# Optimization experiments

Hardware: AMD Instinct MI355X
Metric: run time of the kernel (lower is better)

The kernel has to match this reference:

```python
import jax, jax.numpy as jnp
import numpy as np
from jax import lax

B, N, D = 8, 16384, 64
NPOINT, NSAMPLE, RADIUS = 1024, 32, 0.1
MLP = [3 + D, 64, 64, 128]
BN_EPS = 1e-5


def setup_inputs() -> dict:
    key = jax.random.key(0)
    ks = jax.random.split(key, 8)
    inp = {
        'xyz': jax.random.uniform(ks[0], (B, 3, N), dtype=jnp.float32),
        'points': jax.random.normal(ks[1], (B, D, N), dtype=jnp.float32),
    }
    for i, (cin, cout) in enumerate(zip(MLP[:-1], MLP[1:]), start=1):
        inp[f'w{i}'] = jax.random.normal(ks[1 + i], (cout, cin), dtype=jnp.float32) / np.sqrt(cin)
        inp[f'b{i}'] = jnp.zeros((cout,), jnp.float32)
        inp[f'g{i}'] = jnp.ones((cout,), jnp.float32)
        inp[f'be{i}'] = jnp.zeros((cout,), jnp.float32)
    return inp


def farthest_point_sample(xyz, npoint):
    # xyz: (B, N, 3). Deterministic start at index 0 (torch uses randint).
    b, n, _ = xyz.shape

    def step(carry, _):
        distance, farthest = carry  # (B,N), (B,)
        centroid = jnp.take_along_axis(xyz, farthest[:, None, None], axis=1)  # (B,1,3)
        dist = jnp.sum((xyz - centroid) ** 2, axis=-1)  # (B,N)
        distance = jnp.minimum(distance, dist)
        new_far = jnp.argmax(distance, axis=-1).astype(jnp.int32)
        return (distance, new_far), farthest

    init = (jnp.full((b, n), 1e10, xyz.dtype), jnp.zeros((b,), jnp.int32))
    _, idxs = lax.scan(step, init, None, length=npoint)  # (npoint, B)
    return idxs.T  # (B, npoint)


def query_ball_point(radius, nsample, xyz, new_xyz):
    # xyz: (B,N,3), new_xyz: (B,S,3) -> (B,S,nsample) int32
    b, n, _ = xyz.shape
    # squared pairwise distances (B,S,N)
    sqr = (jnp.sum(new_xyz ** 2, -1)[:, :, None]
           + jnp.sum(xyz ** 2, -1)[:, None, :]
           - 2.0 * jnp.einsum('bsc,bnc->bsn', new_xyz, xyz))
    group_idx = jnp.where(sqr > radius ** 2, n, jnp.arange(n, dtype=jnp.int32))
    group_idx = jnp.sort(group_idx, axis=-1)[:, :, :nsample]
    first = group_idx[:, :, :1]
    return jnp.where(group_idx == n, first, group_idx)


def reference(xyz, points, w1, b1, g1, be1, w2, b2, g2, be2, w3, b3, g3, be3):
    xyz_t = xyz.transpose(0, 2, 1)      # (B,N,3)
    pts_t = points.transpose(0, 2, 1)   # (B,N,D)
    bsz = xyz_t.shape[0]

    fps_idx = farthest_point_sample(xyz_t, NPOINT)          # (B,S)
    bidx2 = jnp.arange(bsz)[:, None]
    new_xyz = xyz_t[bidx2, fps_idx]                          # (B,S,3)

    idx = query_ball_point(RADIUS, NSAMPLE, xyz_t, new_xyz)  # (B,S,ns)
    bidx3 = jnp.arange(bsz)[:, None, None]
    grouped_xyz = xyz_t[bidx3, idx] - new_xyz[:, :, None, :]  # (B,S,ns,3)
    grouped_pts = pts_t[bidx3, idx]                           # (B,S,ns,D)
    feat = jnp.concatenate([grouped_xyz, grouped_pts], axis=-1)  # (B,S,ns,C)

    for w, b, g, be in ((w1, b1, g1, be1), (w2, b2, g2, be2), (w3, b3, g3, be3)):
        feat = jnp.einsum('bsnc,oc->bsno', feat, w) + b
        mean = feat.mean(axis=(0, 1, 2))
        var = feat.var(axis=(0, 1, 2))  # biased, as torch BN uses for normalization
        feat = (feat - mean) * lax.rsqrt(var + BN_EPS) * g + be
        feat = jax.nn.relu(feat)

    new_points = feat.max(axis=2)  # max over nsample -> (B,S,Cout)
    return new_xyz.transpose(0, 2, 1), new_points.transpose(0, 2, 1)
```

## Files before the change

kernel.cpp:

```cpp
#include <hip/hip_runtime.h>
#include <hip/hip_bf16.h>
#include <stdint.h>

#define BATCH 8
#define NPTS  16384
#define DIMF  64
#define SPTS  1024
#define NSAMP 32
#define MTOT  (BATCH*SPTS*NSAMP)

__device__ __forceinline__ float bfu_lo(uint32_t u){ return __uint_as_float(u<<16); }
__device__ __forceinline__ float bfu_hi(uint32_t u){ return __uint_as_float(u & 0xffff0000u); }
__device__ __forceinline__ uint16_t f2bf(float f){
  __hip_bfloat16 h = __float2bfloat16(f);
  uint16_t u; __builtin_memcpy(&u, &h, 2); return u;
}

__global__ __launch_bounds__(256) void transpose_kernel(const float* __restrict__ pts,
                                                        float* __restrict__ ptsT){
  __shared__ float tile[32][33];
  int b = blockIdx.z;
  int n0 = blockIdx.x*32, c0 = blockIdx.y*32;
  int tx = threadIdx.x & 31, ty = threadIdx.x >> 5;
  const float* src = pts + (size_t)b*DIMF*NPTS;
  float* dst = ptsT + (size_t)b*NPTS*DIMF;
#pragma unroll
  for (int j=0;j<4;j++)
    tile[ty+8*j][tx] = src[(size_t)(c0+ty+8*j)*NPTS + n0 + tx];
  __syncthreads();
#pragma unroll
  for (int j=0;j<4;j++)
    dst[(size_t)(n0+ty+8*j)*DIMF + c0 + tx] = tile[tx][ty+8*j];
}

__global__ __launch_bounds__(512, 2) void fps_kernel(const float* __restrict__ xyz,
                                                     float* __restrict__ out0){
  int b = blockIdx.x;
  const float* X = xyz + (size_t)b*3*NPTS;
  int t = threadIdx.x;
  int lane = t & 63, wid = t >> 6;
  float px[32], py[32], pz[32], dst[32];
#pragma unroll
  for (int k=0;k<32;k++){
    int n = t + (k<<9);
    px[k]=X[n]; py[k]=X[NPTS+n]; pz[k]=X[2*NPTS+n];
    dst[k]=1e10f;
  }
  __shared__ float rv[2][8];
  __shared__ int   ri[2][8];
  int far = 0;
  float* o = out0 + (size_t)b*3*SPTS;
  for (int s=0;s<SPTS;s++){
    float cx = X[far], cy = X[NPTS+far], cz = X[2*NPTS+far];
    if (t==0){ o[s]=cx; o[SPTS+s]=cy; o[2*SPTS+s]=cz; }
    if (s==SPTS-1) break;
    float best = -1.0f; int bi = 0x7fffffff;
#pragma unroll
    for (int k=0;k<32;k++){
      float dx=__fsub_rn(px[k],cx), dy=__fsub_rn(py[k],cy), dz=__fsub_rn(pz[k],cz);
      float d = __fadd_rn(__fadd_rn(__fmul_rn(dx,dx),__fmul_rn(dy,dy)),__fmul_rn(dz,dz));
      d = fminf(dst[k], d); dst[k] = d;
      if (d > best){ best = d; bi = t + (k<<9); }
    }
#pragma unroll
    for (int off=1; off<64; off<<=1){
      float ov = __shfl_xor(best, off);
      int   oi = __shfl_xor(bi, off);
      if (ov > best || (ov == best && oi < bi)){ best = ov; bi = oi; }
    }
    int p = s & 1;
    if (lane==0){ rv[p][wid]=best; ri[p][wid]=bi; }
    __syncthreads();
    float v = rv[p][lane&7]; int j = ri[p][lane&7];
#pragma unroll
    for (int off=1; off<8; off<<=1){
      float ov = __shfl_xor(v, off);
      int   oj = __shfl_xor(j, off);
      if (ov > v || (ov == v && oj < j)){ v = ov; j = oj; }
    }
    far = j;
  }
}

__global__ __launch_bounds__(256) void ball_kernel(const float* __restrict__ xyz,
                                                   const float* __restrict__ newxyz,
                                                   int* __restrict__ idxo){
  int b  = blockIdx.x >> 5;
  int sc = blockIdx.x & 31;
  const float* X  = xyz + (size_t)b*3*NPTS;
  int t = threadIdx.x, lane = t & 63, w = t >> 6;
  __shared__ float lx[512], ly[512], lz[512], ls[512];
  __shared__ int done;
  if (t==0) done = 0;
  const float rsq = 0.01f;
  float nx[8], ny[8], nz[8], sn[8];
  int cnt[8], first[8];
  int sbase = sc*32 + w*8;
#pragma unroll
  for (int q=0;q<8;q++){
    int s = sbase + q;
    nx[q] = newxyz[(size_t)b*3*SPTS + s];
    ny[q] = newxyz[(size_t)b*3*SPTS + SPTS + s];
    nz[q] = newxyz[(size_t)b*3*SPTS + 2*SPTS + s];
    sn[q] = __fadd_rn(__fadd_rn(__fmul_rn(nx[q],nx[q]),__fmul_rn(ny[q],ny[q])),
                      __fmul_rn(nz[q],nz[q]));
    cnt[q]=0; first[q]=0;
  }
  __syncthreads();
  for (int T=0;T<32;T++){
    {
      float ax = X[T*512 + t], ay = X[NPTS + T*512 + t], az = X[2*NPTS + T*512 + t];
      lx[t]=ax; ly[t]=ay; lz[t]=az;
      ls[t] = __fadd_rn(__fadd_rn(__fmul_rn(ax,ax),__fmul_rn(ay,ay)),__fmul_rn(az,az));
      float bx = X[T*512 + t + 256], by = X[NPTS + T*512 + t + 256], bz = X[2*NPTS + T*512 + t + 256];
      lx[t+256]=bx; ly[t+256]=by; lz[t+256]=bz;
      ls[t+256] = __fadd_rn(__fadd_rn(__fmul_rn(bx,bx),__fmul_rn(by,by)),__fmul_rn(bz,bz));
    }
    __syncthreads();
#pragma unroll
    for (int q=0;q<8;q++){
      if (cnt[q] >= NSAMP) continue;
      int s = sbase + q;
      int* op = idxo + ((size_t)(b*SPTS + s))*NSAMP;
      for (int c=0;c<8;c++){
        int li = c*64 + lane;
        float dot = fmaf(nz[q], lz[li], fmaf(ny[q], ly[li], __fmul_rn(nx[q], lx[li])));
        float sq  = __fsub_rn(__fadd_rn(sn[q], ls[li]), __fmul_rn(2.0f, dot));
        bool in = (sq <= rsq);
        unsigned long long m = __ballot(in);
        if (cnt[q]==0 && m) first[q] = T*512 + c*64 + (int)__builtin_ctzll(m);
        if (in){
          int slot = cnt[q] + (int)__popcll(m & ((1ull<<lane)-1ull));
          if (slot < NSAMP) op[slot] = T*512 + li;
        }
        cnt[q] += (int)__popcll(m);
        if (cnt[q] >= NSAMP){ if (lane==0) atomicAdd(&done,1); break; }
      }
    }
    __syncthreads();
    if (done >= 32) break;
  }
#pragma unroll
  for (int q=0;q<8;q++){
    if (cnt[q] < NSAMP){
      int s = sbase + q;
      int* op = idxo + ((size_t)(b*SPTS + s))*NSAMP;
      if (lane >= cnt[q] && lane < NSAMP) op[lane] = first[q];
    }
  }
}

__global__ __launch_bounds__(256) void gemm1_kernel(const float* __restrict__ xyz,
                                                    const float* __restrict__ ptsT,
                                                    const int* __restrict__ idx,
                                                    const float* __restrict__ newxyz,
                                                    const float* __restrict__ w1,
                                                    const float* __restrict__ b1,
                                                    uint16_t* __restrict__ y1,
                                                    float* __restrict__ gsum,
                                                    float* __restrict__ gsq){
  __shared__ float As[128*69];
  __shared__ float Ws[67*64];
  __shared__ float bias[64];
  __shared__ int   ndx[128];
  __shared__ float nxs[4][3];
  int t = threadIdx.x;
  int g0 = blockIdx.x*128;
  if (t < 128) ndx[t] = idx[g0 + t];
  if (t < 12){
    int grp = t/3, c = t%3;
    int bs = (g0>>5) + grp; int b = bs>>10, s = bs & 1023;
    nxs[grp][c] = newxyz[(size_t)b*3*SPTS + c*SPTS + s];
  }
  if (t < 64) bias[t] = b1[t];
  for (int e=t; e<67*64; e+=256){ int k=e>>6, c=e&63; Ws[k*64+c] = w1[c*67+k]; }
  __syncthreads();
  {
    int r = t>>1, h = t&1;
    int n = ndx[r];
    int bs = (g0>>5) + (r>>5); int b = bs>>10;
    const float* pr = ptsT + ((size_t)(b*NPTS + n))*64 + h*32;
    float* ar = As + r*69;
    if (h==0){
      int grp = r>>5;
      ar[0] = __fsub_rn(xyz[(size_t)b*3*NPTS + n],          nxs[grp][0]);
      ar[1] = __fsub_rn(xyz[(size_t)b*3*NPTS + NPTS + n],   nxs[grp][1]);
      ar[2] = __fsub_rn(xyz[(size_t)b*3*NPTS + 2*NPTS + n], nxs[grp][2]);
    }
    float* ap = ar + 3 + h*32;
#pragma unroll
    for (int j=0;j<8;j++){
      float4 v = *(const float4*)(pr + j*4);
      ap[j*4+0]=v.x; ap[j*4+1]=v.y; ap[j*4+2]=v.z; ap[j*4+3]=v.w;
    }
  }
  __syncthreads();
  int rg = t>>3, cg = t&7;
  float acc[4][8];
#pragma unroll
  for (int i=0;i<4;i++)
#pragma unroll
    for (int j=0;j<8;j++) acc[i][j]=0.f;
  for (int k=0;k<67;k++){
    float a0 = As[(rg*4+0)*69+k];
    float a1 = As[(rg*4+1)*69+k];
    float a2 = As[(rg*4+2)*69+k];
    float a3 = As[(rg*4+3)*69+k];
    const float* wr = Ws + k*64 + cg*8;
    float4 w0 = *(const float4*)wr;
    float4 w1v = *(const float4*)(wr+4);
    float wj[8] = {w0.x,w0.y,w0.z,w0.w,w1v.x,w1v.y,w1v.z,w1v.w};
#pragma unroll
    for (int j=0;j<8;j++){
      acc[0][j] = fmaf(a0, wj[j], acc[0][j]);
      acc[1][j] = fmaf(a1, wj[j], acc[1][j]);
      acc[2][j] = fmaf(a2, wj[j], acc[2][j]);
      acc[3][j] = fmaf(a3, wj[j], acc[3][j]);
    }
  }
  float ps[8], pq[8];
#pragma unroll
  for (int j=0;j<8;j++){ ps[j]=0.f; pq[j]=0.f; }
#pragma unroll
  for (int i=0;i<4;i++){
    int gr = g0 + rg*4 + i;
    uint16_t* yr = y1 + (size_t)gr*64 + cg*8;
    uint4 vv; uint32_t u[4]; float vj[8];
#pragma unroll
    for (int j=0;j<8;j++){
      vj[j] = acc[i][j] + bias[cg*8+j];
      ps[j] += vj[j]; pq[j] += vj[j]*vj[j];
    }
#pragma unroll
    for (int j=0;j<4;j++)
      u[j] = (uint32_t)f2bf(vj[2*j]) | ((uint32_t)f2bf(vj[2*j+1])<<16);
    vv.x=u[0]; vv.y=u[1]; vv.z=u[2]; vv.w=u[3];
    *(uint4*)yr = vv;
  }
  __syncthreads();
  float* red = As;
#pragma unroll
  for (int j=0;j<8;j++){
    red[rg*65 + cg*8 + j]        = ps[j];
    red[2080 + rg*65 + cg*8 + j] = pq[j];
  }
  __syncthreads();
  if (t < 64){
    float s=0.f, q=0.f;
    for (int r=0;r<32;r++){ s += red[r*65+t]; q += red[2080 + r*65 + t]; }
    atomicAdd(&gsum[t], s); atomicAdd(&gsq[t], q);
  }
}

__global__ __launch_bounds__(256) void gemm2_kernel(const uint16_t* __restrict__ yin,
                                                    const float* __restrict__ w2,
                                                    const float* __restrict__ b2,
                                                    const float* __restrict__ gsumi,
                                                    const float* __restrict__ gsqi,
                                                    const float* __restrict__ gi,
                                                    const float* __restrict__ bei,
                                                    uint16_t* __restrict__ yout,
                                                    float* __restrict__ gsum,
                                                    float* __restrict__ gsq){
  __shared__ float As[128*65];
  __shared__ float Ws[64*64];
  __shared__ float bias[64], sc[64], sh[64];
  int t = threadIdx.x;
  int g0 = blockIdx.x*128;
  if (t < 64){
    bias[t]=b2[t];
    double mean = (double)gsumi[t] / (double)MTOT;
    double var  = (double)gsqi[t] / (double)MTOT - mean*mean;
    double sv   = (double)gi[t] / sqrt(var + 1e-5);
    sc[t] = (float)sv;
    sh[t] = (float)((double)bei[t] - mean*sv);
  }
  for (int e=t; e<64*64; e+=256){ int k=e>>6, c=e&63; Ws[k*64+c] = w2[c*64+k]; }
  __syncthreads();
  {
    int r = t>>1, h = t&1;
    const uint4* yv = (const uint4*)(yin + (size_t)(g0+r)*64 + h*32);
    float* ar = As + r*65 + h*32;
#pragma unroll
    for (int j=0;j<4;j++){
      uint4 u = yv[j];
      uint32_t vv[4] = {u.x,u.y,u.z,u.w};
#pragma unroll
      for (int m=0;m<4;m++){
        int c = h*32 + j*8 + m*2;
        ar[j*8+m*2]   = fmaxf(fmaf(bfu_lo(vv[m]), sc[c],   sh[c]),   0.f);
        ar[j*8+m*2+1] = fmaxf(fmaf(bfu_hi(vv[m]), sc[c+1], sh[c+1]), 0.f);
      }
    }
  }
  __syncthreads();
  int rg = t>>3, cg = t&7;
  float acc[4][8];
#pragma unroll
  for (int i=0;i<4;i++)
#pragma unroll
    for (int j=0;j<8;j++) acc[i][j]=0.f;
  for (int k=0;k<64;k++){
    float a0 = As[(rg*4+0)*65+k];
    float a1 = As[(rg*4+1)*65+k];
    float a2 = As[(rg*4+2)*65+k];
    float a3 = As[(rg*4+3)*65+k];
    const float* wr = Ws + k*64 + cg*8;
    float4 w0 = *(const float4*)wr;
    float4 w1v = *(const float4*)(wr+4);
    float wj[8] = {w0.x,w0.y,w0.z,w0.w,w1v.x,w1v.y,w1v.z,w1v.w};
#pragma unroll
    for (int j=0;j<8;j++){
      acc[0][j] = fmaf(a0, wj[j], acc[0][j]);
      acc[1][j] = fmaf(a1, wj[j], acc[1][j]);
      acc[2][j] = fmaf(a2, wj[j], acc[2][j]);
      acc[3][j] = fmaf(a3, wj[j], acc[3][j]);
    }
  }
  float ps[8], pq[8];
#pragma unroll
  for (int j=0;j<8;j++){ ps[j]=0.f; pq[j]=0.f; }
#pragma unroll
  for (int i=0;i<4;i++){
    int gr = g0 + rg*4 + i;
    uint16_t* yr = yout + (size_t)gr*64 + cg*8;
    uint4 vv; uint32_t u[4]; float vj[8];
#pragma unroll
    for (int j=0;j<8;j++){
      vj[j] = acc[i][j] + bias[cg*8+j];
      ps[j] += vj[j]; pq[j] += vj[j]*vj[j];
    }
#pragma unroll
    for (int j=0;j<4;j++)
      u[j] = (uint32_t)f2bf(vj[2*j]) | ((uint32_t)f2bf(vj[2*j+1])<<16);
    vv.x=u[0]; vv.y=u[1]; vv.z=u[2]; vv.w=u[3];
    *(uint4*)yr = vv;
  }
  __syncthreads();
  float* red = As;
#pragma unroll
  for (int j=0;j<8;j++){
    red[rg*65 + cg*8 + j]        = ps[j];
    red[2080 + rg*65 + cg*8 + j] = pq[j];
  }
  __syncthreads();
  if (t < 64){
    float s=0.f, q=0.f;
    for (int r=0;r<32;r++){ s += red[r*65+t]; q += red[2080 + r*65 + t]; }
    atomicAdd(&gsum[t], s); atomicAdd(&gsq[t], q);
  }
}

__global__ __launch_bounds__(256) void gemm3_kernel(const uint16_t* __restrict__ yin,
                                                    const float* __restrict__ w3,
                                                    const float* __restrict__ b3,
                                                    const float* __restrict__ gsumi,
                                                    const float* __restrict__ gsqi,
                                                    const float* __restrict__ gi,
                                                    const float* __restrict__ bei,
                                                    uint16_t* __restrict__ yout,
                                                    float* __restrict__ gsum,
                                                    float* __restrict__ gsq){
  __shared__ float As[64*65];
  __shared__ float Ws[64*128];
  __shared__ float bias[128], sc[64], sh[64];
  int t = threadIdx.x;
  int g0 = blockIdx.x*64;
  if (t < 128) bias[t]=b3[t];
  if (t < 64){
    double mean = (double)gsumi[t] / (double)MTOT;
    double var  = (double)gsqi[t] / (double)MTOT - mean*mean;
    double sv   = (double)gi[t] / sqrt(var + 1e-5);
    sc[t] = (float)sv;
    sh[t] = (float)((double)bei[t] - mean*sv);
  }
  for (int e=t; e<64*128; e+=256){ int k=e>>7, c=e&127; Ws[k*128+c] = w3[c*64+k]; }
  __syncthreads();
  {
    int r = t>>2, h = t&3;
    const uint4* yv = (const uint4*)(yin + (size_t)(g0+r)*64 + h*16);
    float* ar = As + r*65 + h*16;
#pragma unroll
    for (int j=0;j<2;j++){
      uint4 u = yv[j];
      uint32_t vv[4] = {u.x,u.y,u.z,u.w};
#pragma unroll
      for (int m=0;m<4;m++){
        int c = h*16 + j*8 + m*2;
        ar[j*8+m*2]   = fmaxf(fmaf(bfu_lo(vv[m]), sc[c],   sh[c]),   0.f);
        ar[j*8+m*2+1] = fmaxf(fmaf(bfu_hi(vv[m]), sc[c+1], sh[c+1]), 0.f);
      }
    }
  }
  __syncthreads();
  int rg = t>>4, cg = t&15;
  float acc[4][8];
#pragma unroll
  for (int i=0;i<4;i++)
#pragma unroll
    for (int j=0;j<8;j++) acc[i][j]=0.f;
  for (int k=0;k<64;k++){
    float a0 = As[(rg*4+0)*65+k];
    float a1 = As[(rg*4+1)*65+k];
    float a2 = As[(rg*4+2)*65+k];
    float a3 = As[(rg*4+3)*65+k];
    const float* wr = Ws + k*128 + cg*8;
    float4 w0 = *(const float4*)wr;
    float4 w1v = *(const float4*)(wr+4);
    float wj[8] = {w0.x,w0.y,w0.z,w0.w,w1v.x,w1v.y,w1v.z,w1v.w};
#pragma unroll
    for (int j=0;j<8;j++){
      acc[0][j] = fmaf(a0, wj[j], acc[0][j]);
      acc[1][j] = fmaf(a1, wj[j], acc[1][j]);
      acc[2][j] = fmaf(a2, wj[j], acc[2][j]);
      acc[3][j] = fmaf(a3, wj[j], acc[3][j]);
    }
  }
  float ps[8], pq[8];
#pragma unroll
  for (int j=0;j<8;j++){ ps[j]=0.f; pq[j]=0.f; }
#pragma unroll
  for (int i=0;i<4;i++){
    int gr = g0 + rg*4 + i;
    uint16_t* yr = yout + (size_t)gr*128 + cg*8;
    uint4 vv; uint32_t u[4]; float vj[8];
#pragma unroll
    for (int j=0;j<8;j++){
      vj[j] = acc[i][j] + bias[cg*8+j];
      ps[j] += vj[j]; pq[j] += vj[j]*vj[j];
    }
#pragma unroll
    for (int j=0;j<4;j++)
      u[j] = (uint32_t)f2bf(vj[2*j]) | ((uint32_t)f2bf(vj[2*j+1])<<16);
    vv.x=u[0]; vv.y=u[1]; vv.z=u[2]; vv.w=u[3];
    *(uint4*)yr = vv;
  }
  __syncthreads();
  float* red = As;
#pragma unroll
  for (int j=0;j<8;j++){
    red[rg*129 + cg*8 + j]        = ps[j];
    red[2064 + rg*129 + cg*8 + j] = pq[j];
  }
  __syncthreads();
  if (t < 128){
    float s=0.f, q=0.f;
    for (int r=0;r<16;r++){ s += red[r*129+t]; q += red[2064 + r*129 + t]; }
    atomicAdd(&gsum[t], s); atomicAdd(&gsq[t], q);
  }
}

__global__ __launch_bounds__(256) void maxpool_kernel(const uint16_t* __restrict__ y3,
                                                      const float* __restrict__ gsumi,
                                                      const float* __restrict__ gsqi,
                                                      const float* __restrict__ gi,
                                                      const float* __restrict__ bei,
                                                      float* __restrict__ out1){
  __shared__ float tr[16][129];
  __shared__ float scs[128], shs[128];
  int t = threadIdx.x;
  int b = blockIdx.x >> 6;
  int s0 = (blockIdx.x & 63) * 16;
  if (t < 128){
    double mean = (double)gsumi[t] / (double)MTOT;
    double var  = (double)gsqi[t] / (double)MTOT - mean*mean;
    double sv   = (double)gi[t] / sqrt(var + 1e-5);
    scs[t] = (float)sv;
    shs[t] = (float)((double)bei[t] - mean*sv);
  }
  __syncthreads();
  int ch = t & 127, sl0 = t >> 7;
  float scv = scs[ch], shv = shs[ch];
  for (int sl=sl0; sl<16; sl+=2){
    int bs = b*SPTS + s0 + sl;
    const uint16_t* yr = y3 + (size_t)bs*NSAMP*128 + ch;
    float m = 0.0f;
#pragma unroll 4
    for (int k=0;k<NSAMP;k++){
      float v = __uint_as_float(((uint32_t)yr[k*128])<<16);
      float z = fmaxf(fmaf(v, scv, shv), 0.f);
      m = fmaxf(m, z);
    }
    tr[sl][ch] = m;
  }
  __syncthreads();
  int ch2 = t >> 1, hh = t & 1;
  float vals[8];
#pragma unroll
  for (int i=0;i<8;i++) vals[i] = tr[hh*8+i][ch2];
  float* op = out1 + (size_t)b*131072 + (size_t)ch2*1024 + s0 + hh*8;
  float4 v0; v0.x=vals[0]; v0.y=vals[1]; v0.z=vals[2]; v0.w=vals[3];
  float4 v1; v1.x=vals[4]; v1.y=vals[5]; v1.z=vals[6]; v1.w=vals[7];
  *(float4*)op = v0;
  *(float4*)(op+4) = v1;
}

extern "C" void kernel_launch(void* const* d_in, const int* in_sizes, int n_in,
                              void* d_out, int out_size, void* d_ws, size_t ws_size,
                              hipStream_t stream){
  (void)in_sizes; (void)n_in; (void)out_size; (void)ws_size;
  const float* xyz = (const float*)d_in[0];
  const float* pts = (const float*)d_in[1];
  const float* w1 = (const float*)d_in[2];  const float* b1 = (const float*)d_in[3];
  const float* g1 = (const float*)d_in[4];  const float* be1 = (const float*)d_in[5];
  const float* w2 = (const float*)d_in[6];  const float* b2 = (const float*)d_in[7];
  const float* g2 = (const float*)d_in[8];  const float* be2 = (const float*)d_in[9];
  const float* w3 = (const float*)d_in[10]; const float* b3 = (const float*)d_in[11];
  const float* g3 = (const float*)d_in[12]; const float* be3 = (const float*)d_in[13];

  float* out0 = (float*)d_out;
  float* out1 = out0 + BATCH*3*SPTS;

  char* ws = (char*)d_ws;
  float*    ptsT = (float*)(ws + 0);
  int*      idx  = (int*)  (ws + 34078720);
  uint16_t* y1   = (uint16_t*)(ws + 35127296);
  uint16_t* y2   = (uint16_t*)(ws + 68681728);
  uint16_t* y3   = (uint16_t*)(ws + 102236160);
  float*    stats = (float*)(ws + 169345024);
  float* gsum1 = stats;        float* gsq1 = stats + 128;
  float* gsum2 = stats + 256;  float* gsq2 = stats + 384;
  float* gsum3 = stats + 512;  float* gsq3 = stats + 640;

  hipMemsetAsync(stats, 0, 768*sizeof(float), stream);

  transpose_kernel<<<dim3(NPTS/32, DIMF/32, BATCH), 256, 0, stream>>>(pts, ptsT);
  fps_kernel<<<BATCH, 512, 0, stream>>>(xyz, out0);
  ball_kernel<<<BATCH*32, 256, 0, stream>>>(xyz, out0, idx);
  gemm1_kernel<<<MTOT/128, 256, 0, stream>>>(xyz, ptsT, idx, out0, w1, b1, y1, gsum1, gsq1);
  gemm2_kernel<<<MTOT/128, 256, 0, stream>>>(y1, w2, b2, gsum1, gsq1, g1, be1, y2, gsum2, gsq2);
  gemm3_kernel<<<MTOT/64, 256, 0, stream>>>(y2, w3, b3, gsum2, gsq2, g2, be2, y3, gsum3, gsq3);
  maxpool_kernel<<<BATCH*(SPTS/16), 256, 0, stream>>>(y3, gsum3, gsq3, g3, be3, out1);
}
```

Before: 2.660 ms.

## Fold points transpose into FPS launch and shard BN stat atomics

The standalone transpose kernel is removed and its work is done by extra blocks appended to the FPS launch. Those blocks can run on otherwise idle compute units while the eight serial FPS blocks are busy. The BN sum and sum-of-squares accumulators are split into 16 slots chosen by block index, and consumers add the slots back together, to cut contention on the same global atomics. The cost is a larger memset, a 64x65 shared tile added to the FPS kernel's footprint, and a 16-way reduction in every consumer block.

Result: no change. 2.617 ms (-1.6%).

```diff
diff --git a/kernel.cpp b/kernel.cpp
--- a/kernel.cpp
+++ b/kernel.cpp
@@ -16,25 +16,32 @@
   uint16_t u; __builtin_memcpy(&u, &h, 2); return u;
 }
 
-__global__ __launch_bounds__(256) void transpose_kernel(const float* __restrict__ pts,
-                                                        float* __restrict__ ptsT){
-  __shared__ float tile[32][33];
-  int b = blockIdx.z;
-  int n0 = blockIdx.x*32, c0 = blockIdx.y*32;
-  int tx = threadIdx.x & 31, ty = threadIdx.x >> 5;
-  const float* src = pts + (size_t)b*DIMF*NPTS;
-  float* dst = ptsT + (size_t)b*NPTS*DIMF;
-#pragma unroll
-  for (int j=0;j<4;j++)
-    tile[ty+8*j][tx] = src[(size_t)(c0+ty+8*j)*NPTS + n0 + tx];
-  __syncthreads();
-#pragma unroll
-  for (int j=0;j<4;j++)
-    dst[(size_t)(n0+ty+8*j)*DIMF + c0 + tx] = tile[tx][ty+8*j];
-}
-
 __global__ __launch_bounds__(512, 2) void fps_kernel(const float* __restrict__ xyz,
-                                                     float* __restrict__ out0){
+                                                     float* __restrict__ out0,
+                                                     const float* __restrict__ pts,
+                                                     float* __restrict__ ptsT){
+  if (blockIdx.x >= BATCH){
+    __shared__ float tile[64][65];
+    int bb = blockIdx.x - BATCH;
+    int b  = bb >> 8;
+    int n0 = (bb & 255) << 6;
+    const float* src = pts + (size_t)b*DIMF*NPTS;
+    float* dst = ptsT + (size_t)b*NPTS*DIMF;
+    int t = threadIdx.x;
+    int cn = t & 63, cw = t >> 6;
+#pragma unroll
+    for (int j=0;j<8;j++){
+      int c = cw + j*8;
+      tile[c][cn] = src[(size_t)c*NPTS + n0 + cn];
+    }
+    __syncthreads();
+#pragma unroll
+    for (int j=0;j<8;j++){
+      int nl = cw + j*8;
+      dst[(size_t)(n0+nl)*DIMF + cn] = tile[cn][nl];
+    }
+    return;
+  }
   int b = blockIdx.x;
   const float* X = xyz + (size_t)b*3*NPTS;
   int t = threadIdx.x;
@@ -248,7 +255,8 @@
   if (t < 64){
     float s=0.f, q=0.f;
     for (int r=0;r<32;r++){ s += red[r*65+t]; q += red[2080 + r*65 + t]; }
-    atomicAdd(&gsum[t], s); atomicAdd(&gsq[t], q);
+    int kb = (blockIdx.x & 15) * 128;
+    atomicAdd(&gsum[kb + t], s); atomicAdd(&gsq[kb + t], q);
   }
 }
 
@@ -269,8 +277,10 @@
   int g0 = blockIdx.x*128;
   if (t < 64){
     bias[t]=b2[t];
-    double mean = (double)gsumi[t] / (double)MTOT;
-    double var  = (double)gsqi[t] / (double)MTOT - mean*mean;
+    double ssum=0.0, ssq=0.0;
+    for (int k2=0;k2<16;k2++){ ssum += (double)gsumi[k2*128+t]; ssq += (double)gsqi[k2*128+t]; }
+    double mean = ssum / (double)MTOT;
+    double var  = ssq / (double)MTOT - mean*mean;
     double sv   = (double)gi[t] / sqrt(var + 1e-5);
     sc[t] = (float)sv;
     sh[t] = (float)((double)bei[t] - mean*sv);
@@ -347,7 +357,8 @@
   if (t < 64){
     float s=0.f, q=0.f;
     for (int r=0;r<32;r++){ s += red[r*65+t]; q += red[2080 + r*65 + t]; }
-    atomicAdd(&gsum[t], s); atomicAdd(&gsq[t], q);
+    int kb = (blockIdx.x & 15) * 128;
+    atomicAdd(&gsum[kb + t], s); atomicAdd(&gsq[kb + t], q);
   }
 }
 
@@ -368,8 +379,10 @@
   int g0 = blockIdx.x*64;
   if (t < 128) bias[t]=b3[t];
   if (t < 64){
-    double mean = (double)gsumi[t] / (double)MTOT;
-    double var  = (double)gsqi[t] / (double)MTOT - mean*mean;
+    double ssum=0.0, ssq=0.0;
+    for (int k2=0;k2<16;k2++){ ssum += (double)gsumi[k2*128+t]; ssq += (double)gsqi[k2*128+t]; }
+    double mean = ssum / (double)MTOT;
+    double var  = ssq / (double)MTOT - mean*mean;
     double sv   = (double)gi[t] / sqrt(var + 1e-5);
     sc[t] = (float)sv;
     sh[t] = (float)((double)bei[t] - mean*sv);
@@ -446,7 +459,8 @@
   if (t < 128){
     float s=0.f, q=0.f;
     for (int r=0;r<16;r++){ s += red[r*129+t]; q += red[2064 + r*129 + t]; }
-    atomicAdd(&gsum[t], s); atomicAdd(&gsq[t], q);
+    int kb = (blockIdx.x & 15) * 128;
+    atomicAdd(&gsum[kb + t], s); atomicAdd(&gsq[kb + t], q);
   }
 }
 
@@ -462,8 +476,10 @@
   int b = blockIdx.x >> 6;
   int s0 = (blockIdx.x & 63) * 16;
   if (t < 128){
-    double mean = (double)gsumi[t] / (double)MTOT;
-    double var  = (double)gsqi[t] / (double)MTOT - mean*mean;
+    double ssum=0.0, ssq=0.0;
+    for (int k2=0;k2<16;k2++){ ssum += (double)gsumi[k2*128+t]; ssq += (double)gsqi[k2*128+t]; }
+    double mean = ssum / (double)MTOT;
+    double var  = ssq / (double)MTOT - mean*mean;
     double sv   = (double)gi[t] / sqrt(var + 1e-5);
     scs[t] = (float)sv;
     shs[t] = (float)((double)bei[t] - mean*sv);
@@ -513,19 +529,18 @@
 
   char* ws = (char*)d_ws;
   float*    ptsT = (float*)(ws + 0);
+  float*    stats = (float*)(ws + 33554432);
   int*      idx  = (int*)  (ws + 34078720);
   uint16_t* y1   = (uint16_t*)(ws + 35127296);
   uint16_t* y2   = (uint16_t*)(ws + 68681728);
   uint16_t* y3   = (uint16_t*)(ws + 102236160);
-  float*    stats = (float*)(ws + 169345024);
-  float* gsum1 = stats;        float* gsq1 = stats + 128;
-  float* gsum2 = stats + 256;  float* gsq2 = stats + 384;
-  float* gsum3 = stats + 512;  float* gsq3 = stats + 640;
-
-  hipMemsetAsync(stats, 0, 768*sizeof(float), stream);
-
-  transpose_kernel<<<dim3(NPTS/32, DIMF/32, BATCH), 256, 0, stream>>>(pts, ptsT);
-  fps_kernel<<<BATCH, 512, 0, stream>>>(xyz, out0);
+  float* gsum1 = stats;          float* gsq1 = stats + 2048;
+  float* gsum2 = stats + 4096;   float* gsq2 = stats + 6144;
+  float* gsum3 = stats + 8192;   float* gsq3 = stats + 10240;
+
+  hipMemsetAsync(stats, 0, 12288*sizeof(float), stream);
+
+  fps_kernel<<<BATCH + 2048, 512, 0, stream>>>(xyz, out0, pts, ptsT);
   ball_kernel<<<BATCH*32, 256, 0, stream>>>(xyz, out0, idx);
   gemm1_kernel<<<MTOT/128, 256, 0, stream>>>(xyz, ptsT, idx, out0, w1, b1, y1, gsum1, gsq1);
   gemm2_kernel<<<MTOT/128, 256, 0, stream>>>(y1, w2, b2, gsum1, gsq1, g1, be1, y2, gsum2, gsq2);
```
